# Kernel tuning notes

Hardware: AMD Instinct MI355X
Metric: run time of the kernel (lower is better)

Reference implementation:

```python
import jax, jax.numpy as jnp
import numpy as np

HEADS = 16
D_MODEL = 1024
D_HEAD = D_MODEL // HEADS


def setup_inputs() -> dict:
    key = jax.random.key(0)
    ks = jax.random.split(key, 9)
    s_h = 1.0 / np.sqrt(D_HEAD)
    s_m = 1.0 / np.sqrt(D_MODEL)
    return {
        "x": jax.random.normal(ks[0], (4, 2048, D_MODEL), dtype=jnp.float32),
        "Wq": jax.random.uniform(ks[1], (D_HEAD, D_HEAD), jnp.float32, -s_h, s_h),
        "bq": jax.random.uniform(ks[2], (D_HEAD,), jnp.float32, -s_h, s_h),
        "Wk": jax.random.uniform(ks[3], (D_HEAD, D_HEAD), jnp.float32, -s_h, s_h),
        "bk": jax.random.uniform(ks[4], (D_HEAD,), jnp.float32, -s_h, s_h),
        "Wv": jax.random.uniform(ks[5], (D_HEAD, D_HEAD), jnp.float32, -s_h, s_h),
        "bv": jax.random.uniform(ks[6], (D_HEAD,), jnp.float32, -s_h, s_h),
        "Wp": jax.random.uniform(ks[7], (D_MODEL, D_MODEL), jnp.float32, -s_m, s_m),
        "bp": jax.random.uniform(ks[8], (D_MODEL,), jnp.float32, -s_m, s_m),
    }


def reference(x, Wq, bq, Wk, bk, Wv, bv, Wp, bp):
    B, T, C = x.shape
    xh = x.reshape(B, T, HEADS, D_HEAD)  # [B,T,H,Dh]
    # per-head linear projections (torch Linear: x @ W.T + b)
    q = jnp.einsum('bthd,ed->bhte', xh, Wq) + bq  # [B,H,T,Dh]
    k = jnp.einsum('bthd,ed->bhte', xh, Wk) + bk
    v = jnp.einsum('bthd,ed->bhte', xh, Wv) + bv
    # NOTE: original scales by sqrt(C) = sqrt(d_model), not sqrt(d_head)
    att = jnp.einsum('bhqd,bhkd->bhqk', q, k) / jnp.sqrt(jnp.float32(C))
    att = jax.nn.softmax(att, axis=-1)
    out = jnp.einsum('bhqk,bhkd->bhqd', att, v)  # [B,H,T,Dh]
    out = out.transpose(0, 2, 1, 3).reshape(B, T, C)
    return out @ Wp.T + bp
```

## Files before the change

kernel.cpp:

```cpp
#include <hip/hip_runtime.h>
#include <hip/hip_bf16.h>
#include <cstddef>

#define B_  4
#define T_  2048
#define H_  16
#define DH  64
#define C_  1024
#define BH  64

typedef float  f32x16 __attribute__((ext_vector_type(16)));
typedef __bf16 bf16x8 __attribute__((ext_vector_type(8)));

#define MFMA32(a, b, c) __builtin_amdgcn_mfma_f32_32x32x16_bf16(a, b, c, 0, 0, 0)


__global__ __launch_bounds__(256) void qkv_kernel(
    const float* __restrict__ x,
    const float* __restrict__ Wq, const float* __restrict__ bq,
    const float* __restrict__ Wk, const float* __restrict__ bk,
    const float* __restrict__ Wv, const float* __restrict__ bv,
    __bf16* __restrict__ q, __bf16* __restrict__ k, __bf16* __restrict__ vt)
{
    __shared__ __bf16 Xs[128 * 72];
    __shared__ __bf16 Ws[3][64 * 72];
    __bf16* Vtl = Xs;

    const int tt  = blockIdx.x;
    const int bh  = blockIdx.y;
    const int b   = bh >> 4, h = bh & 15;
    const int t0  = tt * 128;
    const int tid = threadIdx.x;
    const int wave = tid >> 6, lane = tid & 63;
    const int m = lane & 31, hh = lane >> 5;

    #pragma unroll
    for (int i = 0; i < 8; ++i) {
        const int idx = i * 256 + tid;
        const int r = idx >> 4, c = (idx & 15) * 4;
        const float4 x4 = *(const float4*)(x + ((size_t)(b * T_ + t0 + r)) * C_ + h * DH + c);
        const uint lo = ((uint)__builtin_bit_cast(unsigned short, (__bf16)x4.y) << 16)
                      | (uint)__builtin_bit_cast(unsigned short, (__bf16)x4.x);
        const uint hi = ((uint)__builtin_bit_cast(unsigned short, (__bf16)x4.w) << 16)
                      | (uint)__builtin_bit_cast(unsigned short, (__bf16)x4.z);
        *(uint*)&Xs[r * 72 + c]     = lo;
        *(uint*)&Xs[r * 72 + c + 2] = hi;
    }
    #pragma unroll
    for (int i = 0; i < 4; ++i) {
        const int idx = i * 256 + tid;
        const int r = idx >> 4, c = (idx & 15) * 4;
        const float* wsrc[3] = {Wq, Wk, Wv};
        #pragma unroll
        for (int wv_ = 0; wv_ < 3; ++wv_) {
            const float4 w4 = *(const float4*)(wsrc[wv_] + r * 64 + c);
            const uint lo = ((uint)__builtin_bit_cast(unsigned short, (__bf16)w4.y) << 16)
                          | (uint)__builtin_bit_cast(unsigned short, (__bf16)w4.x);
            const uint hi = ((uint)__builtin_bit_cast(unsigned short, (__bf16)w4.w) << 16)
                          | (uint)__builtin_bit_cast(unsigned short, (__bf16)w4.z);
            *(uint*)&Ws[wv_][r * 72 + c]     = lo;
            *(uint*)&Ws[wv_][r * 72 + c + 2] = hi;
        }
    }
    __syncthreads();

    bf16x8 xf[4];
    #pragma unroll
    for (int ks = 0; ks < 4; ++ks)
        xf[ks] = *(const bf16x8*)&Xs[(wave * 32 + m) * 72 + ks * 16 + hh * 8];
    __syncthreads();

    const float s32 = 0.03125f;

    #pragma unroll
    for (int mat = 0; mat < 3; ++mat) {
        f32x16 acc0 = {}, acc1 = {};
        #pragma unroll
        for (int ks = 0; ks < 4; ++ks) {
            const bf16x8 w0 = *(const bf16x8*)&Ws[mat][(m) * 72 + ks * 16 + hh * 8];
            const bf16x8 w1 = *(const bf16x8*)&Ws[mat][(32 + m) * 72 + ks * 16 + hh * 8];
            acc0 = MFMA32(xf[ks], w0, acc0);
            acc1 = MFMA32(xf[ks], w1, acc1);
        }
        const float* bias = (mat == 0) ? bq : (mat == 1) ? bk : bv;
        const float b0 = bias[m], b1 = bias[32 + m];
        #pragma unroll
        for (int r = 0; r < 16; ++r) {
            const int R = (r & 3) + 8 * (r >> 2) + 4 * hh;
            const int tloc = wave * 32 + R;
            const float v0 = acc0[r] + b0, v1 = acc1[r] + b1;
            if (mat == 0) {
                const size_t base = ((size_t)bh * T_ + t0 + tloc) * DH;
                q[base + m]      = (__bf16)(v0 * s32);
                q[base + 32 + m] = (__bf16)(v1 * s32);
            } else if (mat == 1) {
                const size_t base = ((size_t)bh * T_ + t0 + tloc) * DH;
                k[base + m]      = (__bf16)v0;
                k[base + 32 + m] = (__bf16)v1;
            } else {
                Vtl[(m) * 136 + tloc]      = (__bf16)v0;
                Vtl[(32 + m) * 136 + tloc] = (__bf16)v1;
            }
        }
    }
    __syncthreads();
    #pragma unroll
    for (int i = 0; i < 4; ++i) {
        const int idx = i * 256 + tid;
        const int e = idx >> 4, c = (idx & 15) * 8;
        *(uint4*)(vt + ((size_t)(bh * 64 + e)) * T_ + t0 + c) = *(uint4*)&Vtl[e * 136 + c];
    }
}

__global__ __launch_bounds__(256, 3) void attn_kernel(
    const __bf16* __restrict__ q, const __bf16* __restrict__ k,
    const __bf16* __restrict__ vt, __bf16* __restrict__ o)
{
    __shared__ __bf16 Ks[64 * 72];
    __shared__ __bf16 Vts[64 * 72];
    __shared__ __bf16 Ps[128 * 72];

    const int bh  = blockIdx.y;
    const int q0  = blockIdx.x * 128;
    const int tid = threadIdx.x;
    const int wave = tid >> 6, lane = tid & 63;
    const int m = lane & 31, h = lane >> 5;
    const int qrow0 = wave * 32;

    const __bf16* qb = q  + (size_t)bh * T_ * DH;
    const __bf16* kb = k  + (size_t)bh * T_ * DH;
    const __bf16* vb = vt + (size_t)bh * DH * T_;

    #pragma unroll
    for (int i = 0; i < 4; ++i) {
        const int idx = i * 256 + tid;
        const int r = idx >> 3, c = (idx & 7) * 8;
        *(uint4*)&Ps[r * 72 + c] = *(const uint4*)(qb + (size_t)(q0 + r) * DH + c);
    }
    __syncthreads();

    bf16x8 qf[4];
    #pragma unroll
    for (int ks = 0; ks < 4; ++ks)
        qf[ks] = *(const bf16x8*)&Ps[(qrow0 + m) * 72 + ks * 16 + h * 8];

    f32x16 O0 = {}, O1 = {};
    float lsum[16];
    #pragma unroll
    for (int r = 0; r < 16; ++r) lsum[r] = 0.f;

    for (int kt = 0; kt < T_; kt += 64) {
        __syncthreads();
        #pragma unroll
        for (int i = 0; i < 2; ++i) {
            const int idx = i * 256 + tid;
            const int r = idx >> 3, c = (idx & 7) * 8;
            *(uint4*)&Ks[r * 72 + c] = *(const uint4*)(kb + (size_t)(kt + r) * DH + c);
        }
        #pragma unroll
        for (int i = 0; i < 2; ++i) {
            const int idx = i * 256 + tid;
            const int r = idx >> 3, c = (idx & 7) * 8;
            *(uint4*)&Vts[r * 72 + c] = *(const uint4*)(vb + (size_t)r * T_ + kt + c);
        }
        __syncthreads();

        f32x16 S0 = {}, S1 = {};
        #pragma unroll
        for (int ks = 0; ks < 4; ++ks) {
            const bf16x8 k0 = *(const bf16x8*)&Ks[(m) * 72 + ks * 16 + h * 8];
            const bf16x8 k1 = *(const bf16x8*)&Ks[(32 + m) * 72 + ks * 16 + h * 8];
            S0 = MFMA32(qf[ks], k0, S0);
            S1 = MFMA32(qf[ks], k1, S1);
        }

        #pragma unroll
        for (int r = 0; r < 16; ++r) {
            const int R = (r & 3) + 8 * (r >> 2) + 4 * h;
            const float p0 = __expf(S0[r]);
            const float p1 = __expf(S1[r]);
            lsum[r] += p0 + p1;
            Ps[(qrow0 + R) * 72 + m]      = (__bf16)p0;
            Ps[(qrow0 + R) * 72 + 32 + m] = (__bf16)p1;
        }

        #pragma unroll
        for (int ks = 0; ks < 4; ++ks) {
            const bf16x8 pf = *(const bf16x8*)&Ps[(qrow0 + m) * 72 + ks * 16 + h * 8];
            const bf16x8 v0 = *(const bf16x8*)&Vts[(m) * 72 + ks * 16 + h * 8];
            const bf16x8 v1 = *(const bf16x8*)&Vts[(32 + m) * 72 + ks * 16 + h * 8];
            O0 = MFMA32(pf, v0, O0);
            O1 = MFMA32(pf, v1, O1);
        }
    }

    #pragma unroll
    for (int r = 0; r < 16; ++r) {
        float s = lsum[r];
        s += __shfl_xor(s, 1);  s += __shfl_xor(s, 2);  s += __shfl_xor(s, 4);
        s += __shfl_xor(s, 8);  s += __shfl_xor(s, 16);
        lsum[r] = 1.0f / s;
    }
    __bf16* ob = o + (size_t)bh * T_ * DH;
    #pragma unroll
    for (int r = 0; r < 16; ++r) {
        const int R = (r & 3) + 8 * (r >> 2) + 4 * h;
        const size_t row = (size_t)(q0 + qrow0 + R) * DH;
        ob[row + m]      = (__bf16)(O0[r] * lsum[r]);
        ob[row + 32 + m] = (__bf16)(O1[r] * lsum[r]);
    }
}

__global__ __launch_bounds__(256) void proj_kernel(
    const __bf16* __restrict__ a,
    const float* __restrict__ Wp, const float* __restrict__ bp,
    float* __restrict__ out)
{
    __shared__ __bf16 As[128 * 72];
    __shared__ __bf16 Bs[128 * 72];

    const int tb = blockIdx.x, eb = blockIdx.y;
    const int tid = threadIdx.x;
    const int wave = tid >> 6, lane = tid & 63;
    const int m = lane & 31, h = lane >> 5;
    const int tok0 = tb * 128;
    const int b = tok0 >> 11, t0 = tok0 & (T_ - 1);
    const int e0 = eb * 128;

    f32x16 acc[4] = {f32x16{}, f32x16{}, f32x16{}, f32x16{}};

    for (int cb = 0; cb < 16; ++cb) {
        __syncthreads();
        #pragma unroll
        for (int i = 0; i < 4; ++i) {
            const int idx = i * 256 + tid;
            const int r = idx >> 3, c = (idx & 7) * 8;
            *(uint4*)&As[r * 72 + c] =
                *(const uint4*)(a + ((size_t)(b * H_ + cb) * T_ + t0 + r) * DH + c);
        }
        #pragma unroll
        for (int i = 0; i < 8; ++i) {
            const int idx = i * 256 + tid;
            const int r = idx >> 4, c = (idx & 15) * 4;
            const float4 w4 = *(const float4*)(Wp + (size_t)(e0 + r) * C_ + cb * 64 + c);
            const uint lo = ((uint)__builtin_bit_cast(unsigned short, (__bf16)w4.y) << 16)
                          | (uint)__builtin_bit_cast(unsigned short, (__bf16)w4.x);
            const uint hi = ((uint)__builtin_bit_cast(unsigned short, (__bf16)w4.w) << 16)
                          | (uint)__builtin_bit_cast(unsigned short, (__bf16)w4.z);
            *(uint*)&Bs[r * 72 + c]     = lo;
            *(uint*)&Bs[r * 72 + c + 2] = hi;
        }
        __syncthreads();

        #pragma unroll
        for (int ks = 0; ks < 4; ++ks) {
            const bf16x8 af = *(const bf16x8*)&As[(wave * 32 + m) * 72 + ks * 16 + h * 8];
            #pragma unroll
            for (int n = 0; n < 4; ++n) {
                const bf16x8 bf = *(const bf16x8*)&Bs[(n * 32 + m) * 72 + ks * 16 + h * 8];
                acc[n] = MFMA32(af, bf, acc[n]);
            }
        }
    }

    #pragma unroll
    for (int n = 0; n < 4; ++n) {
        const int e = e0 + n * 32 + m;
        const float bias = bp[e];
        #pragma unroll
        for (int r = 0; r < 16; ++r) {
            const int R = (r & 3) + 8 * (r >> 2) + 4 * h;
            out[(size_t)(tok0 + wave * 32 + R) * C_ + e] = acc[n][r] + bias;
        }
    }
}

extern "C" void kernel_launch(void* const* d_in, const int* in_sizes, int n_in,
                              void* d_out, int out_size, void* d_ws, size_t ws_size,
                              hipStream_t stream)
{
    const float* x  = (const float*)d_in[0];
    const float* Wq = (const float*)d_in[1];
    const float* bq = (const float*)d_in[2];
    const float* Wk = (const float*)d_in[3];
    const float* bk = (const float*)d_in[4];
    const float* Wv = (const float*)d_in[5];
    const float* bv = (const float*)d_in[6];
    const float* Wp = (const float*)d_in[7];
    const float* bp = (const float*)d_in[8];

    const size_t N = (size_t)BH * T_ * DH;
    __bf16* qws  = (__bf16*)d_ws;
    __bf16* kws  = qws + N;
    __bf16* vtws = kws + N;
    __bf16* ows  = vtws + N;

    qkv_kernel<<<dim3(16, 64), 256, 0, stream>>>(
        x, Wq, bq, Wk, bk, Wv, bv, qws, kws, vtws);
    attn_kernel<<<dim3(16, 64), 256, 0, stream>>>(qws, kws, vtws, ows);
    proj_kernel<<<dim3(64, 8), 256, 0, stream>>>(ows, Wp, bp, (float*)d_out);
}
```

Measured before the change: 234.1 us.

## Keep softmax P in registers via transposed MFMA and prefetch K/V tiles

The attention kernel now computes S transposed (K as the A operand), so the exponentiated probabilities can be packed to bf16 with v_cvt_pk_bf16 and rearranged with v_permlane32_swap. They feed the PV MFMA directly, removing the Ps shared-memory round trip. K/V tiles for the next step are prefetched into registers while the current tile is being computed, and the scale folds log2(e) into Q so exp2 can replace expf. Occupancy is raised to 4 blocks per SM, and output stores become vectorized bf16x4. The cost is higher register pressure and reliance on gfx950-specific inline asm.

```diff
diff --git a/kernel.cpp b/kernel.cpp
--- a/kernel.cpp
+++ b/kernel.cpp
@@ -11,9 +11,16 @@
 
 typedef float  f32x16 __attribute__((ext_vector_type(16)));
 typedef __bf16 bf16x8 __attribute__((ext_vector_type(8)));
+typedef __bf16 bf16x4 __attribute__((ext_vector_type(4)));
 
 #define MFMA32(a, b, c) __builtin_amdgcn_mfma_f32_32x32x16_bf16(a, b, c, 0, 0, 0)
 
+
+__device__ __forceinline__ unsigned cvt_pk_bf16(float lo, float hi) {
+    unsigned r;
+    asm("v_cvt_pk_bf16_f32 %0, %1, %2" : "=v"(r) : "v"(lo), "v"(hi));
+    return r;
+}
 
 __global__ __launch_bounds__(256) void qkv_kernel(
     const float* __restrict__ x,
@@ -39,12 +46,12 @@
         const int idx = i * 256 + tid;
         const int r = idx >> 4, c = (idx & 15) * 4;
         const float4 x4 = *(const float4*)(x + ((size_t)(b * T_ + t0 + r)) * C_ + h * DH + c);
-        const uint lo = ((uint)__builtin_bit_cast(unsigned short, (__bf16)x4.y) << 16)
-                      | (uint)__builtin_bit_cast(unsigned short, (__bf16)x4.x);
-        const uint hi = ((uint)__builtin_bit_cast(unsigned short, (__bf16)x4.w) << 16)
-                      | (uint)__builtin_bit_cast(unsigned short, (__bf16)x4.z);
-        *(uint*)&Xs[r * 72 + c]     = lo;
-        *(uint*)&Xs[r * 72 + c + 2] = hi;
+        const unsigned lo = ((unsigned)__builtin_bit_cast(unsigned short, (__bf16)x4.y) << 16)
+                          | (unsigned)__builtin_bit_cast(unsigned short, (__bf16)x4.x);
+        const unsigned hi = ((unsigned)__builtin_bit_cast(unsigned short, (__bf16)x4.w) << 16)
+                          | (unsigned)__builtin_bit_cast(unsigned short, (__bf16)x4.z);
+        *(unsigned*)&Xs[r * 72 + c]     = lo;
+        *(unsigned*)&Xs[r * 72 + c + 2] = hi;
     }
     #pragma unroll
     for (int i = 0; i < 4; ++i) {
@@ -54,12 +61,12 @@
         #pragma unroll
         for (int wv_ = 0; wv_ < 3; ++wv_) {
             const float4 w4 = *(const float4*)(wsrc[wv_] + r * 64 + c);
-            const uint lo = ((uint)__builtin_bit_cast(unsigned short, (__bf16)w4.y) << 16)
-                          | (uint)__builtin_bit_cast(unsigned short, (__bf16)w4.x);
-            const uint hi = ((uint)__builtin_bit_cast(unsigned short, (__bf16)w4.w) << 16)
-                          | (uint)__builtin_bit_cast(unsigned short, (__bf16)w4.z);
-            *(uint*)&Ws[wv_][r * 72 + c]     = lo;
-            *(uint*)&Ws[wv_][r * 72 + c + 2] = hi;
+            const unsigned lo = ((unsigned)__builtin_bit_cast(unsigned short, (__bf16)w4.y) << 16)
+                              | (unsigned)__builtin_bit_cast(unsigned short, (__bf16)w4.x);
+            const unsigned hi = ((unsigned)__builtin_bit_cast(unsigned short, (__bf16)w4.w) << 16)
+                              | (unsigned)__builtin_bit_cast(unsigned short, (__bf16)w4.z);
+            *(unsigned*)&Ws[wv_][r * 72 + c]     = lo;
+            *(unsigned*)&Ws[wv_][r * 72 + c + 2] = hi;
         }
     }
     __syncthreads();
@@ -70,7 +77,7 @@
         xf[ks] = *(const bf16x8*)&Xs[(wave * 32 + m) * 72 + ks * 16 + hh * 8];
     __syncthreads();
 
-    const float s32 = 0.03125f;
+    const float s32 = 0.03125f * 1.4426950408889634f;
 
     #pragma unroll
     for (int mat = 0; mat < 3; ++mat) {
@@ -112,13 +119,12 @@
     }
 }
 
-__global__ __launch_bounds__(256, 3) void attn_kernel(
+__global__ __launch_bounds__(256, 4) void attn_kernel(
     const __bf16* __restrict__ q, const __bf16* __restrict__ k,
     const __bf16* __restrict__ vt, __bf16* __restrict__ o)
 {
     __shared__ __bf16 Ks[64 * 72];
     __shared__ __bf16 Vts[64 * 72];
-    __shared__ __bf16 Ps[128 * 72];
 
     const int bh  = blockIdx.y;
     const int q0  = blockIdx.x * 128;
@@ -131,83 +137,100 @@
     const __bf16* kb = k  + (size_t)bh * T_ * DH;
     const __bf16* vb = vt + (size_t)bh * DH * T_;
 
-    #pragma unroll
-    for (int i = 0; i < 4; ++i) {
-        const int idx = i * 256 + tid;
-        const int r = idx >> 3, c = (idx & 7) * 8;
-        *(uint4*)&Ps[r * 72 + c] = *(const uint4*)(qb + (size_t)(q0 + r) * DH + c);
-    }
-    __syncthreads();
-
     bf16x8 qf[4];
     #pragma unroll
     for (int ks = 0; ks < 4; ++ks)
-        qf[ks] = *(const bf16x8*)&Ps[(qrow0 + m) * 72 + ks * 16 + h * 8];
+        qf[ks] = *(const bf16x8*)(qb + (size_t)(q0 + qrow0 + m) * DH + ks * 16 + h * 8);
+
+    const int r0s = tid >> 3;
+    const int c0s = (tid & 7) * 8;
+
+    uint4 kreg[2], vreg[2];
+    #pragma unroll
+    for (int i = 0; i < 2; ++i) {
+        kreg[i] = *(const uint4*)(kb + (size_t)(r0s + 32 * i) * DH + c0s);
+        vreg[i] = *(const uint4*)(vb + (size_t)(r0s + 32 * i) * T_ + c0s);
+    }
+    #pragma unroll
+    for (int i = 0; i < 2; ++i) {
+        *(uint4*)&Ks[(r0s + 32 * i) * 72 + c0s]  = kreg[i];
+        *(uint4*)&Vts[(r0s + 32 * i) * 72 + c0s] = vreg[i];
+    }
 
     f32x16 O0 = {}, O1 = {};
-    float lsum[16];
-    #pragma unroll
-    for (int r = 0; r < 16; ++r) lsum[r] = 0.f;
+    float lsum = 0.f;
 
     for (int kt = 0; kt < T_; kt += 64) {
         __syncthreads();
-        #pragma unroll
-        for (int i = 0; i < 2; ++i) {
-            const int idx = i * 256 + tid;
-            const int r = idx >> 3, c = (idx & 7) * 8;
-            *(uint4*)&Ks[r * 72 + c] = *(const uint4*)(kb + (size_t)(kt + r) * DH + c);
-        }
-        #pragma unroll
-        for (int i = 0; i < 2; ++i) {
-            const int idx = i * 256 + tid;
-            const int r = idx >> 3, c = (idx & 7) * 8;
-            *(uint4*)&Vts[r * 72 + c] = *(const uint4*)(vb + (size_t)r * T_ + kt + c);
-        }
-        __syncthreads();
+        const bool pre = (kt + 64 < T_);
+        if (pre) {
+            #pragma unroll
+            for (int i = 0; i < 2; ++i) {
+                kreg[i] = *(const uint4*)(kb + (size_t)(kt + 64 + r0s + 32 * i) * DH + c0s);
+                vreg[i] = *(const uint4*)(vb + (size_t)(r0s + 32 * i) * T_ + kt + 64 + c0s);
+            }
+        }
 
         f32x16 S0 = {}, S1 = {};
         #pragma unroll
         for (int ks = 0; ks < 4; ++ks) {
             const bf16x8 k0 = *(const bf16x8*)&Ks[(m) * 72 + ks * 16 + h * 8];
             const bf16x8 k1 = *(const bf16x8*)&Ks[(32 + m) * 72 + ks * 16 + h * 8];
-            S0 = MFMA32(qf[ks], k0, S0);
-            S1 = MFMA32(qf[ks], k1, S1);
-        }
-
-        #pragma unroll
-        for (int r = 0; r < 16; ++r) {
-            const int R = (r & 3) + 8 * (r >> 2) + 4 * h;
-            const float p0 = __expf(S0[r]);
-            const float p1 = __expf(S1[r]);
-            lsum[r] += p0 + p1;
-            Ps[(qrow0 + R) * 72 + m]      = (__bf16)p0;
-            Ps[(qrow0 + R) * 72 + 32 + m] = (__bf16)p1;
-        }
-
-        #pragma unroll
-        for (int ks = 0; ks < 4; ++ks) {
-            const bf16x8 pf = *(const bf16x8*)&Ps[(qrow0 + m) * 72 + ks * 16 + h * 8];
-            const bf16x8 v0 = *(const bf16x8*)&Vts[(m) * 72 + ks * 16 + h * 8];
-            const bf16x8 v1 = *(const bf16x8*)&Vts[(32 + m) * 72 + ks * 16 + h * 8];
-            O0 = MFMA32(pf, v0, O0);
-            O1 = MFMA32(pf, v1, O1);
-        }
-    }
-
-    #pragma unroll
-    for (int r = 0; r < 16; ++r) {
-        float s = lsum[r];
-        s += __shfl_xor(s, 1);  s += __shfl_xor(s, 2);  s += __shfl_xor(s, 4);
-        s += __shfl_xor(s, 8);  s += __shfl_xor(s, 16);
-        lsum[r] = 1.0f / s;
-    }
-    __bf16* ob = o + (size_t)bh * T_ * DH;
-    #pragma unroll
-    for (int r = 0; r < 16; ++r) {
-        const int R = (r & 3) + 8 * (r >> 2) + 4 * h;
-        const size_t row = (size_t)(q0 + qrow0 + R) * DH;
-        ob[row + m]      = (__bf16)(O0[r] * lsum[r]);
-        ob[row + 32 + m] = (__bf16)(O1[r] * lsum[r]);
+            S0 = MFMA32(k0, qf[ks], S0);
+            S1 = MFMA32(k1, qf[ks], S1);
+        }
+
+        #pragma unroll
+        for (int c = 0; c < 4; ++c) {
+            const f32x16 Sh = (c < 2) ? S0 : S1;
+            const int rb = (c & 1) * 8;
+            float e0 = __builtin_amdgcn_exp2f(Sh[rb + 0]);
+            float e1 = __builtin_amdgcn_exp2f(Sh[rb + 1]);
+            float e2 = __builtin_amdgcn_exp2f(Sh[rb + 2]);
+            float e3 = __builtin_amdgcn_exp2f(Sh[rb + 3]);
+            float e4 = __builtin_amdgcn_exp2f(Sh[rb + 4]);
+            float e5 = __builtin_amdgcn_exp2f(Sh[rb + 5]);
+            float e6 = __builtin_amdgcn_exp2f(Sh[rb + 6]);
+            float e7 = __builtin_amdgcn_exp2f(Sh[rb + 7]);
+            lsum += ((e0 + e1) + (e2 + e3)) + ((e4 + e5) + (e6 + e7));
+            unsigned a0 = cvt_pk_bf16(e0, e1);
+            unsigned a1 = cvt_pk_bf16(e2, e3);
+            unsigned b0 = cvt_pk_bf16(e4, e5);
+            unsigned b1 = cvt_pk_bf16(e6, e7);
+            asm("v_permlane32_swap_b32 %0, %1" : "+v"(a0), "+v"(b0));
+            asm("v_permlane32_swap_b32 %0, %1" : "+v"(a1), "+v"(b1));
+            const uint4 pw = {a0, a1, b0, b1};
+            const bf16x8 pb = __builtin_bit_cast(bf16x8, pw);
+            const bf16x8 va0 = *(const bf16x8*)&Vts[(m) * 72 + c * 16 + h * 8];
+            const bf16x8 va1 = *(const bf16x8*)&Vts[(32 + m) * 72 + c * 16 + h * 8];
+            O0 = MFMA32(va0, pb, O0);
+            O1 = MFMA32(va1, pb, O1);
+        }
+
+        __syncthreads();
+        if (pre) {
+            #pragma unroll
+            for (int i = 0; i < 2; ++i) {
+                *(uint4*)&Ks[(r0s + 32 * i) * 72 + c0s]  = kreg[i];
+                *(uint4*)&Vts[(r0s + 32 * i) * 72 + c0s] = vreg[i];
+            }
+        }
+    }
+
+    lsum += __shfl_xor(lsum, 32);
+    const float linv = 1.0f / lsum;
+
+    __bf16* ob = o + ((size_t)bh * T_ + q0 + qrow0 + m) * DH;
+    #pragma unroll
+    for (int g = 0; g < 4; ++g) {
+        bf16x4 w0, w1;
+        #pragma unroll
+        for (int j = 0; j < 4; ++j) {
+            w0[j] = (__bf16)(O0[4 * g + j] * linv);
+            w1[j] = (__bf16)(O1[4 * g + j] * linv);
+        }
+        *(bf16x4*)(ob + 8 * g + 4 * h)      = w0;
+        *(bf16x4*)(ob + 32 + 8 * g + 4 * h) = w1;
     }
 }
 
@@ -243,12 +266,12 @@
             const int idx = i * 256 + tid;
             const int r = idx >> 4, c = (idx & 15) * 4;
             const float4 w4 = *(const float4*)(Wp + (size_t)(e0 + r) * C_ + cb * 64 + c);
-            const uint lo = ((uint)__builtin_bit_cast(unsigned short, (__bf16)w4.y) << 16)
-                          | (uint)__builtin_bit_cast(unsigned short, (__bf16)w4.x);
-            const uint hi = ((uint)__builtin_bit_cast(unsigned short, (__bf16)w4.w) << 16)
-                          | (uint)__builtin_bit_cast(unsigned short, (__bf16)w4.z);
-            *(uint*)&Bs[r * 72 + c]     = lo;
-            *(uint*)&Bs[r * 72 + c + 2] = hi;
+            const unsigned lo = ((unsigned)__builtin_bit_cast(unsigned short, (__bf16)w4.y) << 16)
+                              | (unsigned)__builtin_bit_cast(unsigned short, (__bf16)w4.x);
+            const unsigned hi = ((unsigned)__builtin_bit_cast(unsigned short, (__bf16)w4.w) << 16)
+                              | (unsigned)__builtin_bit_cast(unsigned short, (__bf16)w4.z);
+            *(unsigned*)&Bs[r * 72 + c]     = lo;
+            *(unsigned*)&Bs[r * 72 + c + 2] = hi;
         }
         __syncthreads();
 
```

New measurement: 287.2 us. 1.23x slower.
